# Optimization experiments

Measured on AMD Instinct MI355X. Metric: run time of the kernel, lower is better.

Reference implementation:

```python
import jax, jax.numpy as jnp
import numpy as np

N = 50000   # nodes
E = 400000  # edges
IN = 64     # input feature dim
H = 4       # heads (layers 1-2)
C = 128     # hidden channels per head
NEG_SLOPE = 0.2


def gat_conv(x, W, a_src, a_dst, b, src, dst, num_nodes):
    """PyG-style GATConv (add_self_loops=False, dropout inactive / eval mode).
    x: [N, F_in]; W: [F_in, H*C]; a_src/a_dst: [H, C]; b: [H*C].
    Returns concat-over-heads output [N, H*C]."""
    h = (x @ W).reshape(num_nodes, a_src.shape[0], a_src.shape[1])  # [N,H,C]
    alpha_s = jnp.einsum('nhc,hc->nh', h, a_src)  # [N,H]
    alpha_d = jnp.einsum('nhc,hc->nh', h, a_dst)  # [N,H]
    e = jax.nn.leaky_relu(alpha_s[src] + alpha_d[dst], NEG_SLOPE)  # [E,H]
    # numerically-stable segment softmax over incoming edges of each dst node
    m = jax.ops.segment_max(e, dst, num_segments=num_nodes)       # [N,H]
    m = jnp.where(jnp.isfinite(m), m, 0.0)                        # empty segments
    p = jnp.exp(e - m[dst])                                       # [E,H]
    denom = jax.ops.segment_sum(p, dst, num_segments=num_nodes)   # [N,H]
    alpha = p / (denom[dst] + 1e-16)                              # [E,H]
    # message = alpha * h[src], scatter-add into dst
    out = jax.ops.segment_sum(alpha[:, :, None] * h[src], dst,
                              num_segments=num_nodes)             # [N,H,C]
    return out.reshape(num_nodes, -1) + b


def setup_inputs() -> dict:
    key = jax.random.key(0)
    ks = jax.random.split(key, 16)
    s = 0.1  # weight scale for stability
    inp = {
        'x': jax.random.normal(ks[0], (N, IN), dtype=jnp.float32),
        'edge_index': jax.random.randint(ks[1], (2, E), 0, N, dtype=jnp.int64),
        # layer 1: 64 -> H*C
        'W1': s * jax.random.normal(ks[2], (IN, H * C), dtype=jnp.float32),
        'a_src1': s * jax.random.normal(ks[3], (H, C), dtype=jnp.float32),
        'a_dst1': s * jax.random.normal(ks[4], (H, C), dtype=jnp.float32),
        'b1': jnp.zeros((H * C,), dtype=jnp.float32),
        # layer 2: H*C -> H*C
        'W2': s * jax.random.normal(ks[5], (H * C, H * C), dtype=jnp.float32),
        'a_src2': s * jax.random.normal(ks[6], (H, C), dtype=jnp.float32),
        'a_dst2': s * jax.random.normal(ks[7], (H, C), dtype=jnp.float32),
        'b2': jnp.zeros((H * C,), dtype=jnp.float32),
        # layer 3: H*C -> C (heads=1)
        'W3': s * jax.random.normal(ks[8], (H * C, C), dtype=jnp.float32),
        'a_src3': s * jax.random.normal(ks[9], (1, C), dtype=jnp.float32),
        'a_dst3': s * jax.random.normal(ks[10], (1, C), dtype=jnp.float32),
        'b3': jnp.zeros((C,), dtype=jnp.float32),
    }
    return inp


def reference(x, edge_index, W1, a_src1, a_dst1, b1, W2, a_src2, a_dst2, b2,
              W3, a_src3, a_dst3, b3):
    src, dst = edge_index[0], edge_index[1]
    h = jax.nn.elu(gat_conv(x, W1, a_src1, a_dst1, b1, src, dst, N))
    h = jax.nn.elu(gat_conv(h, W2, a_src2, a_dst2, b2, src, dst, N))
    h = jax.nn.elu(gat_conv(h, W3, a_src3, a_dst3, b3, src, dst, N))
    return h  # [N, C]
```

## Files before the change

### kernel.cpp

```cpp
#include <hip/hip_runtime.h>
#include <math.h>


#define LRELU_SLOPE 0.2f
#define MPAD 50048

typedef __attribute__((ext_vector_type(8))) short short8;
typedef __attribute__((ext_vector_type(4))) float f32x4;

__device__ __forceinline__ float bf2f(unsigned short u) {
    return __uint_as_float(((unsigned int)u) << 16);
}
__device__ __forceinline__ unsigned short f2bf(float f) {
    unsigned int u = __float_as_uint(f);
    unsigned int r = u + 0x7FFFu + ((u >> 16) & 1u);
    return (unsigned short)(r >> 16);
}
__device__ __forceinline__ void load16_to_lds(const void* g, void* l) {
    __builtin_amdgcn_global_load_lds(
        (const __attribute__((address_space(1))) void*)g,
        (__attribute__((address_space(3))) void*)l, 16, 0, 0);
}
__device__ __forceinline__ float lrelu(float e) {
    return e > 0.f ? e : LRELU_SLOPE * e;
}


__global__ __launch_bounds__(256) void prep_kernel(
    const float* __restrict__ x, const float* __restrict__ W1,
    const float* __restrict__ W2, const float* __restrict__ W3,
    unsigned short* __restrict__ x_bf, unsigned short* __restrict__ W1t,
    unsigned short* __restrict__ W2t, unsigned short* __restrict__ W3t,
    int* __restrict__ counts, int N)
{
    int i = blockIdx.x * 256 + threadIdx.x;
    const int nx = N * 64;
    if (i < nx) { x_bf[i] = f2bf(x[i]); return; }
    i -= nx;
    if (i < 64 * 512) {
        int k = i / 512, nn = i % 512;
        W1t[nn * 64 + k] = f2bf(W1[i]);
        return;
    }
    i -= 64 * 512;
    if (i < 512 * 512) {
        int k = i / 512, nn = i % 512;
        W2t[nn * 512 + k] = f2bf(W2[i]);
        return;
    }
    i -= 512 * 512;
    if (i < 512 * 128) {
        int k = i / 128, nn = i % 128;
        W3t[(size_t)nn * 512 + k] = f2bf(W3[i]);
        return;
    }
    i -= 512 * 128;
    if (i < N) counts[i] = 0;
}


__global__ void count_deg_kernel(const int* __restrict__ dst, int* __restrict__ counts, int E) {
    int e = blockIdx.x * blockDim.x + threadIdx.x;
    if (e < E) atomicAdd(&counts[dst[e]], 1);
}

__global__ __launch_bounds__(1024) void scan1_kernel(const int* __restrict__ counts,
                                                     int* __restrict__ row_ptr,
                                                     int* __restrict__ partial, int n) {
    __shared__ int wsum[16];
    const int t = threadIdx.x;
    const int lane = t & 63, w = t >> 6;
    const int i = blockIdx.x * 1024 + t;
    int v = (i < n) ? counts[i] : 0;
    int s = v;
    #pragma unroll
    for (int off = 1; off < 64; off <<= 1) {
        int u = __shfl_up(s, off);
        if (lane >= off) s += u;
    }
    if (lane == 63) wsum[w] = s;
    __syncthreads();
    if (w == 0 && lane < 16) {
        int tv = wsum[lane];
        #pragma unroll
        for (int off = 1; off < 16; off <<= 1) {
            int u = __shfl_up(tv, off);
            if (lane >= off) tv += u;
        }
        wsum[lane] = tv;
    }
    __syncthreads();
    int incl = s + (w > 0 ? wsum[w - 1] : 0);
    if (i < n) row_ptr[i + 1] = incl;
    if (t == 0) partial[blockIdx.x] = wsum[15];
}

__global__ void scan2_kernel(int* __restrict__ partial, int nb) {
    int lane = threadIdx.x;
    int v = (lane < nb) ? partial[lane] : 0;
    int s = v;
    #pragma unroll
    for (int off = 1; off < 64; off <<= 1) {
        int u = __shfl_up(s, off);
        if (lane >= off) s += u;
    }
    if (lane < nb) partial[lane] = s - v;
}

__global__ __launch_bounds__(1024) void scan3c_kernel(int* __restrict__ row_ptr,
                                                      const int* __restrict__ partial,
                                                      const int* __restrict__ counts,
                                                      int* __restrict__ cursor, int n) {
    const int i = blockIdx.x * 1024 + threadIdx.x;
    if (i < n) {
        int rp1 = row_ptr[i + 1] + partial[blockIdx.x];
        row_ptr[i + 1] = rp1;
        cursor[i] = rp1 - counts[i];
    }
    if (i == 0) row_ptr[0] = 0;
}

__global__ void fill_csr_kernel(const int* __restrict__ src, const int* __restrict__ dst,
                                int* __restrict__ cursor, int* __restrict__ csr_src, int E) {
    int e = blockIdx.x * blockDim.x + threadIdx.x;
    if (e < E) {
        int d = dst[e];
        int pos = atomicAdd(&cursor[d], 1);
        csr_src[pos] = src[e];
    }
}


__global__ __launch_bounds__(256) void gemm_mfma_kernel(
    const unsigned short* __restrict__ A,
    const unsigned short* __restrict__ Bt,
    unsigned short* __restrict__ C,
    const float* __restrict__ a_src,
    const float* __restrict__ a_dst,
    float* __restrict__ als,
    float* __restrict__ ald,
    int M, int N, int K, int H)
{
    __shared__ short As[2 * 128 * 32];
    __shared__ short Bs[2 * 128 * 32];
    const int t = threadIdx.x;
    const int w = t >> 6, lane = t & 63;
    const int wr = w >> 1, wc = w & 1;

    const int nwg = gridDim.x * gridDim.y;
    const int wg  = blockIdx.x + gridDim.x * blockIdx.y;
    const int qch = nwg >> 3, rch = nwg & 7;
    const int xcd = wg & 7, pos = wg >> 3;
    const int lg  = (xcd < rch ? xcd * (qch + 1) : rch * (qch + 1) + (xcd - rch) * qch) + pos;
    const int bx  = lg % gridDim.x;
    const int by  = lg / gridDim.x;

    const int rowBase = by * 128;
    const int colBase = bx * 128;
    const int q = lane >> 4;
    const int r16 = lane & 15;
    const int qs = (q ^ ((r16 >> 1) & 3)) * 8;

    f32x4 acc[4][4] = {};

    const int sRow = t >> 2;
    const int sOff = ((t & 3) ^ ((sRow >> 1) & 3)) * 8;

    const int NT = K >> 5;
    auto stage = [&](int kt, int b) {
        const int koff = kt * 32 + sOff;
        #pragma unroll
        for (int rr = 0; rr < 2; ++rr) {
            const unsigned short* gA = A + (size_t)(rowBase + rr * 64 + sRow) * K + koff;
            load16_to_lds(gA, (char*)As + b * 8192 + rr * 4096 + w * 1024);
            const unsigned short* gB = Bt + (size_t)(colBase + rr * 64 + sRow) * K + koff;
            load16_to_lds(gB, (char*)Bs + b * 8192 + rr * 4096 + w * 1024);
        }
    };

    stage(0, 0);
    __syncthreads();

    for (int kt = 0; kt < NT; ++kt) {
        const int cur = kt & 1;
        if (kt + 1 < NT) stage(kt + 1, cur ^ 1);

        const short* Ab = As + cur * 4096;
        const short* Bb = Bs + cur * 4096;
        short8 af[4], bfr[4];
        #pragma unroll
        for (int m = 0; m < 4; ++m)
            af[m] = *(const short8*)&Ab[(wr * 64 + m * 16 + r16) * 32 + qs];
        #pragma unroll
        for (int n = 0; n < 4; ++n)
            bfr[n] = *(const short8*)&Bb[(wc * 64 + n * 16 + r16) * 32 + qs];
        #pragma unroll
        for (int m = 0; m < 4; ++m)
            #pragma unroll
            for (int n = 0; n < 4; ++n)
                acc[m][n] = __builtin_amdgcn_mfma_f32_16x16x32_bf16(af[m], bfr[n], acc[m][n], 0, 0, 0);

        __syncthreads();
    }

    float asv[4], adv[4];
    #pragma unroll
    for (int n = 0; n < 4; ++n) {
        int col = colBase + wc * 64 + n * 16 + r16;
        asv[n] = a_src[col];
        adv[n] = a_dst[col];
    }
    const int head = bx;

    float* red = (float*)As;

    #pragma unroll
    for (int m = 0; m < 4; ++m) {
        #pragma unroll
        for (int r = 0; r < 4; ++r) {
            const int rowl = wr * 64 + m * 16 + q * 4 + r;
            const int gr = rowBase + rowl;
            float ps = 0.f, pd = 0.f;
            #pragma unroll
            for (int n = 0; n < 4; ++n) {
                ps += acc[m][n][r] * asv[n];
                pd += acc[m][n][r] * adv[n];
            }
            #pragma unroll
            for (int off = 8; off >= 1; off >>= 1) {
                ps += __shfl_xor(ps, off);
                pd += __shfl_xor(pd, off);
            }
            if (r16 == 0) {
                red[wc * 128 + rowl] = ps;
                red[256 + wc * 128 + rowl] = pd;
            }
            if (gr < M) {
                #pragma unroll
                for (int n = 0; n < 4; ++n)
                    C[(size_t)gr * N + colBase + wc * 64 + n * 16 + r16] = f2bf(acc[m][n][r]);
            }
        }
    }
    __syncthreads();
    if (t < 128) {
        const int gr = rowBase + t;
        if (gr < M) {
            als[(size_t)gr * H + head] = red[t] + red[128 + t];
            ald[(size_t)gr * H + head] = red[256 + t] + red[384 + t];
        }
    }
}


__global__ __launch_bounds__(256) void gather4f_kernel(
    const unsigned short* __restrict__ hfeat,
    const float* __restrict__ als, const float* __restrict__ ald,
    const int* __restrict__ row_ptr, const int* __restrict__ csr_src,
    const float* __restrict__ bias, unsigned short* __restrict__ out,
    int n_nodes)
{
    const int lane = threadIdx.x & 63;
    const int wv = threadIdx.x >> 6;
    const int n = blockIdx.x * 4 + wv;
    if (n >= n_nodes) return;
    const int head = lane >> 4;
    const int li = lane & 15;
    const int grpBase = lane & ~15;

    const int start = row_ptr[n];
    const int deg = row_ptr[n + 1] - start;
    const float aldv = ald[(size_t)n * 4 + head];

    float acc[8] = {};
    float wsum = 0.f;
    for (int base = 0; base < deg; base += 16) {
        const int cnt = min(16, deg - base);
        int s_l = 0; float w_l = 0.f;
        if (li < cnt) {
            s_l = csr_src[start + base + li];
            float e = als[(size_t)s_l * 4 + head] + aldv;
            w_l = __expf(lrelu(e));
            wsum += w_l;
        }
        for (int e = 0; e < cnt; ++e) {
            const int s = __shfl(s_l, grpBase + e);
            const float a = __shfl(w_l, grpBase + e);
            short8 v = *(const short8*)(hfeat + (size_t)s * 512 + lane * 8);
            #pragma unroll
            for (int j = 0; j < 8; ++j) acc[j] += a * bf2f((unsigned short)v[j]);
        }
    }

    #pragma unroll
    for (int off = 8; off >= 1; off >>= 1) wsum += __shfl_xor(wsum, off);
    const float sc = (deg > 0) ? 1.f / wsum : 0.f;

    float ov[8];
    #pragma unroll
    for (int j = 0; j < 8; ++j) {
        float o = acc[j] * sc + bias[lane * 8 + j];
        ov[j] = o > 0.f ? o : expm1f(o);
    }
    short8 v;
    #pragma unroll
    for (int j = 0; j < 8; ++j) v[j] = (short)f2bf(ov[j]);
    *(short8*)&out[(size_t)n * 512 + lane * 8] = v;
}


__global__ __launch_bounds__(256) void gather1f_kernel(
    const unsigned short* __restrict__ hfeat,
    const float* __restrict__ als, const float* __restrict__ ald,
    const int* __restrict__ row_ptr, const int* __restrict__ csr_src,
    const float* __restrict__ bias, float* __restrict__ out, int n_nodes)
{
    const int lane = threadIdx.x & 63;
    const int wv = threadIdx.x >> 6;
    const int n = blockIdx.x * 4 + wv;
    if (n >= n_nodes) return;
    const int qid = lane >> 4;
    const int ql = lane & 15;

    const int start = row_ptr[n];
    const int deg = row_ptr[n + 1] - start;
    const float aldv = ald[n];

    float acc[8] = {};
    float wsum = 0.f;
    for (int base = 0; base < deg; base += 64) {
        const int cnt = min(64, deg - base);
        int s_l = 0; float w_l = 0.f;
        if (lane < cnt) {
            s_l = csr_src[start + base + lane];
            float e = als[s_l] + aldv;
            w_l = __expf(lrelu(e));
            wsum += w_l;
        }
        for (int e = 0; e < cnt; e += 4) {
            const int idx = e + qid;
            const int idxc = idx < cnt ? idx : 0;
            const int s = __shfl(s_l, idxc);
            const float aw = __shfl(w_l, idxc);
            const float a = idx < cnt ? aw : 0.f;
            short8 v = *(const short8*)(hfeat + (size_t)s * 128 + ql * 8);
            #pragma unroll
            for (int j = 0; j < 8; ++j) acc[j] += a * bf2f((unsigned short)v[j]);
        }
    }

    #pragma unroll
    for (int off = 32; off >= 1; off >>= 1) wsum += __shfl_xor(wsum, off);
    const float sc = (deg > 0) ? 1.f / wsum : 0.f;

    #pragma unroll
    for (int j = 0; j < 8; ++j) {
        acc[j] += __shfl_xor(acc[j], 16);
        acc[j] += __shfl_xor(acc[j], 32);
    }

    if (qid == 0) {
        float tmp[8];
        #pragma unroll
        for (int j = 0; j < 8; ++j) {
            float o = acc[j] * sc + bias[ql * 8 + j];
            tmp[j] = o > 0.f ? o : expm1f(o);
        }
        float4 o0 = {tmp[0], tmp[1], tmp[2], tmp[3]};
        float4 o1 = {tmp[4], tmp[5], tmp[6], tmp[7]};
        float* op = out + (size_t)n * 128 + ql * 8;
        *(float4*)op = o0;
        *(float4*)(op + 4) = o1;
    }
}


extern "C" void kernel_launch(void* const* d_in, const int* in_sizes, int n_in,
                              void* d_out, int out_size, void* d_ws, size_t ws_size,
                              hipStream_t stream) {
    const float* x   = (const float*)d_in[0];
    const int*   ei  = (const int*)d_in[1];
    const float* W1  = (const float*)d_in[2];
    const float* as1 = (const float*)d_in[3];
    const float* ad1 = (const float*)d_in[4];
    const float* b1  = (const float*)d_in[5];
    const float* W2  = (const float*)d_in[6];
    const float* as2 = (const float*)d_in[7];
    const float* ad2 = (const float*)d_in[8];
    const float* b2  = (const float*)d_in[9];
    const float* W3  = (const float*)d_in[10];
    const float* as3 = (const float*)d_in[11];
    const float* ad3 = (const float*)d_in[12];
    const float* b3  = (const float*)d_in[13];

    const int N = in_sizes[0] / 64;
    const int E = in_sizes[1] / 2;
    const int HC = 512;

    const int* src = ei;
    const int* dst = ei + E;

    size_t off = 0;
    auto carve = [&](size_t bytes) -> void* {
        void* p = (char*)d_ws + off;
        off += (bytes + 255) & ~(size_t)255;
        return p;
    };
    unsigned short* x_bf    = (unsigned short*)carve((size_t)MPAD * 64 * 2);
    unsigned short* feat_bf = (unsigned short*)carve((size_t)MPAD * HC * 2);
    unsigned short* h_bf    = (unsigned short*)carve((size_t)N * HC * 2);
    unsigned short* W1t     = (unsigned short*)carve((size_t)512 * 64 * 2);
    unsigned short* W2t     = (unsigned short*)carve((size_t)512 * 512 * 2);
    unsigned short* W3t     = (unsigned short*)carve((size_t)128 * 512 * 2);
    float* stats  = (float*)carve((size_t)N * 8 * sizeof(float));
    float* als    = stats;
    float* ald    = stats + (size_t)N * 4;
    int*   counts = (int*)carve((size_t)N * sizeof(int));
    int*   row_ptr= (int*)carve((size_t)(N + 1) * sizeof(int));
    int*   cursor = (int*)carve((size_t)N * sizeof(int));
    int*   csr_src= (int*)carve((size_t)E * sizeof(int));
    int*   partial= (int*)carve(64 * sizeof(int));
    (void)ws_size;

    const int nb = (N + 1023) / 1024;
    const int prepTotal = N * 64 + 64 * 512 + 512 * 512 + 512 * 128 + N;

    prep_kernel<<<(prepTotal + 255) / 256, 256, 0, stream>>>(
        x, W1, W2, W3, x_bf, W1t, W2t, W3t, counts, N);

    count_deg_kernel<<<(E + 255) / 256, 256, 0, stream>>>(dst, counts, E);
    scan1_kernel<<<nb, 1024, 0, stream>>>(counts, row_ptr, partial, N);
    scan2_kernel<<<1, 64, 0, stream>>>(partial, nb);
    scan3c_kernel<<<nb, 1024, 0, stream>>>(row_ptr, partial, counts, cursor, N);
    fill_csr_kernel<<<(E + 255) / 256, 256, 0, stream>>>(src, dst, cursor, csr_src, E);

    const int rowTiles = (N + 127) / 128;
    const int aggBlocks = (N + 3) / 4;

    gemm_mfma_kernel<<<dim3(4, rowTiles), 256, 0, stream>>>(x_bf, W1t, h_bf, as1, ad1,
                                                            als, ald, N, 512, 64, 4);
    gather4f_kernel<<<aggBlocks, 256, 0, stream>>>(h_bf, als, ald, row_ptr, csr_src,
                                                   b1, feat_bf, N);

    gemm_mfma_kernel<<<dim3(4, rowTiles), 256, 0, stream>>>(feat_bf, W2t, h_bf, as2, ad2,
                                                            als, ald, N, 512, 512, 4);
    gather4f_kernel<<<aggBlocks, 256, 0, stream>>>(h_bf, als, ald, row_ptr, csr_src,
                                                   b2, feat_bf, N);

    gemm_mfma_kernel<<<dim3(1, rowTiles), 256, 0, stream>>>(feat_bf, W3t, h_bf, as3, ad3,
                                                            als, ald, N, 128, 512, 1);
    gather1f_kernel<<<aggBlocks, 256, 0, stream>>>(h_bf, als, ald, row_ptr, csr_src,
                                                   b3, (float*)d_out, N);
}
```

Measured before the change: 359.4 us.

## Reorder layer-1 GAT to aggregate 64-dim inputs before projecting through W1

```diff
diff --git a/kernel.cpp b/kernel.cpp
--- a/kernel.cpp
+++ b/kernel.cpp
@@ -8,8 +8,8 @@
 typedef __attribute__((ext_vector_type(8))) short short8;
 typedef __attribute__((ext_vector_type(4))) float f32x4;
 
-__device__ __forceinline__ float bf2f(unsigned short u) {
-    return __uint_as_float(((unsigned int)u) << 16);
+__device__ __forceinline__ float bf2f(unsigned int u) {
+    return __uint_as_float(u << 16);
 }
 __device__ __forceinline__ unsigned short f2bf(float f) {
     unsigned int u = __float_as_uint(f);
@@ -29,9 +29,10 @@
 __global__ __launch_bounds__(256) void prep_kernel(
     const float* __restrict__ x, const float* __restrict__ W1,
     const float* __restrict__ W2, const float* __restrict__ W3,
+    const float* __restrict__ as1, const float* __restrict__ ad1,
     unsigned short* __restrict__ x_bf, unsigned short* __restrict__ W1t,
     unsigned short* __restrict__ W2t, unsigned short* __restrict__ W3t,
-    int* __restrict__ counts, int N)
+    int* __restrict__ counts, float* __restrict__ ws, int N)
 {
     int i = blockIdx.x * 256 + threadIdx.x;
     const int nx = N * 64;
@@ -55,7 +56,19 @@
         return;
     }
     i -= 512 * 128;
-    if (i < N) counts[i] = 0;
+    if (i < N) { counts[i] = 0; return; }
+    i -= N;
+    if (i < 256) {
+        int h = i >> 6, k = i & 63;
+        float ss = 0.f, sd = 0.f;
+        for (int c = 0; c < 128; ++c) {
+            float wv = W1[k * 512 + h * 128 + c];
+            ss += wv * as1[h * 128 + c];
+            sd += wv * ad1[h * 128 + c];
+        }
+        ws[i] = ss;
+        ws[256 + i] = sd;
+    }
 }
 
 
@@ -127,6 +140,178 @@
         int d = dst[e];
         int pos = atomicAdd(&cursor[d], 1);
         csr_src[pos] = src[e];
+    }
+}
+
+
+__global__ __launch_bounds__(256) void als1_kernel(const float* __restrict__ x,
+                                                   const float* __restrict__ ws,
+                                                   float* __restrict__ als,
+                                                   float* __restrict__ ald, int n_nodes) {
+    const int lane = threadIdx.x & 63;
+    const int wv = threadIdx.x >> 6;
+    const int n = blockIdx.x * 4 + wv;
+    if (n >= n_nodes) return;
+    const float xv = x[(size_t)n * 64 + lane];
+    float d0 = xv * ws[lane],        d1 = xv * ws[64 + lane];
+    float d2 = xv * ws[128 + lane],  d3 = xv * ws[192 + lane];
+    float e0 = xv * ws[256 + lane],  e1 = xv * ws[320 + lane];
+    float e2 = xv * ws[384 + lane],  e3 = xv * ws[448 + lane];
+    #pragma unroll
+    for (int off = 32; off >= 1; off >>= 1) {
+        d0 += __shfl_xor(d0, off); d1 += __shfl_xor(d1, off);
+        d2 += __shfl_xor(d2, off); d3 += __shfl_xor(d3, off);
+        e0 += __shfl_xor(e0, off); e1 += __shfl_xor(e1, off);
+        e2 += __shfl_xor(e2, off); e3 += __shfl_xor(e3, off);
+    }
+    if (lane == 0) {
+        float4 a = {d0, d1, d2, d3};
+        float4 b = {e0, e1, e2, e3};
+        *(float4*)&als[(size_t)n * 4] = a;
+        *(float4*)&ald[(size_t)n * 4] = b;
+    }
+}
+
+
+__global__ __launch_bounds__(256) void gatherx_kernel(
+    const unsigned short* __restrict__ x_bf,
+    const float* __restrict__ als, const float* __restrict__ ald,
+    const int* __restrict__ row_ptr, const int* __restrict__ csr_src,
+    unsigned short* __restrict__ xagg,
+    int n_nodes)
+{
+    const int lane = threadIdx.x & 63;
+    const int wv = threadIdx.x >> 6;
+    const int n = blockIdx.x * 4 + wv;
+    if (n >= n_nodes) return;
+    const int head = lane >> 4;
+    const int li = lane & 15;
+    const int grpBase = lane & ~15;
+
+    const int start = row_ptr[n];
+    const int deg = row_ptr[n + 1] - start;
+    const float aldv = ald[(size_t)n * 4 + head];
+
+    float acc[4] = {};
+    float wsum = 0.f;
+    for (int base = 0; base < deg; base += 16) {
+        const int cnt = min(16, deg - base);
+        int s_l = 0; float w_l = 0.f;
+        if (li < cnt) {
+            s_l = csr_src[start + base + li];
+            w_l = __expf(lrelu(als[(size_t)s_l * 4 + head] + aldv));
+            wsum += w_l;
+        }
+        for (int e = 0; e < cnt; ++e) {
+            const int s = __shfl(s_l, grpBase + e);
+            const float a = __shfl(w_l, grpBase + e);
+            uint2 v = *(const uint2*)(x_bf + (size_t)s * 64 + li * 4);
+            acc[0] += a * bf2f(v.x & 0xFFFFu);
+            acc[1] += a * bf2f(v.x >> 16);
+            acc[2] += a * bf2f(v.y & 0xFFFFu);
+            acc[3] += a * bf2f(v.y >> 16);
+        }
+    }
+
+    #pragma unroll
+    for (int off = 8; off >= 1; off >>= 1) wsum += __shfl_xor(wsum, off);
+    const float sc = (deg > 0) ? 1.f / wsum : 0.f;
+
+    uint2 o;
+    o.x = (unsigned int)f2bf(acc[0] * sc) | ((unsigned int)f2bf(acc[1] * sc) << 16);
+    o.y = (unsigned int)f2bf(acc[2] * sc) | ((unsigned int)f2bf(acc[3] * sc) << 16);
+    *(uint2*)&xagg[(size_t)n * 256 + head * 64 + li * 4] = o;
+}
+
+
+__global__ __launch_bounds__(256) void gemm_out_kernel(
+    const unsigned short* __restrict__ A,
+    const unsigned short* __restrict__ Bt,
+    const float* __restrict__ bias,
+    unsigned short* __restrict__ Cout,
+    int M)
+{
+    __shared__ short As[2 * 128 * 32];
+    __shared__ short Bs[2 * 128 * 32];
+    const int t = threadIdx.x;
+    const int w = t >> 6, lane = t & 63;
+    const int wr = w >> 1, wc = w & 1;
+
+    const int nwg = gridDim.x * gridDim.y;
+    const int wg  = blockIdx.x + gridDim.x * blockIdx.y;
+    const int qch = nwg >> 3, rch = nwg & 7;
+    const int xcd = wg & 7, pos = wg >> 3;
+    const int lg  = (xcd < rch ? xcd * (qch + 1) : rch * (qch + 1) + (xcd - rch) * qch) + pos;
+    const int bx  = lg % gridDim.x;
+    const int by  = lg / gridDim.x;
+
+    const int rowBase = by * 128;
+    const int head = bx;
+    const int colBase = bx * 128;
+    const int q = lane >> 4;
+    const int r16 = lane & 15;
+    const int qs = (q ^ ((r16 >> 1) & 3)) * 8;
+
+    f32x4 acc[4][4] = {};
+
+    const int sRow = t >> 2;
+    const int sOff = ((t & 3) ^ ((sRow >> 1) & 3)) * 8;
+
+    auto stage = [&](int kt, int b) {
+        const int koff = kt * 32 + sOff;
+        #pragma unroll
+        for (int rr = 0; rr < 2; ++rr) {
+            const unsigned short* gA = A + (size_t)(rowBase + rr * 64 + sRow) * 256 + head * 64 + koff;
+            load16_to_lds(gA, (char*)As + b * 8192 + rr * 4096 + w * 1024);
+            const unsigned short* gB = Bt + (size_t)(colBase + rr * 64 + sRow) * 64 + koff;
+            load16_to_lds(gB, (char*)Bs + b * 8192 + rr * 4096 + w * 1024);
+        }
+    };
+
+    stage(0, 0);
+    __syncthreads();
+
+    #pragma unroll
+    for (int kt = 0; kt < 2; ++kt) {
+        const int cur = kt & 1;
+        if (kt + 1 < 2) stage(kt + 1, cur ^ 1);
+
+        const short* Ab = As + cur * 4096;
+        const short* Bb = Bs + cur * 4096;
+        short8 af[4], bfr[4];
+        #pragma unroll
+        for (int m = 0; m < 4; ++m)
+            af[m] = *(const short8*)&Ab[(wr * 64 + m * 16 + r16) * 32 + qs];
+        #pragma unroll
+        for (int n = 0; n < 4; ++n)
+            bfr[n] = *(const short8*)&Bb[(wc * 64 + n * 16 + r16) * 32 + qs];
+        #pragma unroll
+        for (int m = 0; m < 4; ++m)
+            #pragma unroll
+            for (int n = 0; n < 4; ++n)
+                acc[m][n] = __builtin_amdgcn_mfma_f32_16x16x32_bf16(af[m], bfr[n], acc[m][n], 0, 0, 0);
+
+        __syncthreads();
+    }
+
+    float bv[4];
+    #pragma unroll
+    for (int n = 0; n < 4; ++n) bv[n] = bias[colBase + wc * 64 + n * 16 + r16];
+
+    #pragma unroll
+    for (int m = 0; m < 4; ++m) {
+        #pragma unroll
+        for (int r = 0; r < 4; ++r) {
+            const int gr = rowBase + wr * 64 + m * 16 + q * 4 + r;
+            if (gr < M) {
+                #pragma unroll
+                for (int n = 0; n < 4; ++n) {
+                    float o = acc[m][n][r] + bv[n];
+                    o = o > 0.f ? o : expm1f(o);
+                    Cout[(size_t)gr * 512 + colBase + wc * 64 + n * 16 + r16] = f2bf(o);
+                }
+            }
+        }
     }
 }
 
@@ -288,7 +473,7 @@
             const float a = __shfl(w_l, grpBase + e);
             short8 v = *(const short8*)(hfeat + (size_t)s * 512 + lane * 8);
             #pragma unroll
-            for (int j = 0; j < 8; ++j) acc[j] += a * bf2f((unsigned short)v[j]);
+            for (int j = 0; j < 8; ++j) acc[j] += a * bf2f((unsigned int)(unsigned short)v[j]);
         }
     }
 
@@ -345,7 +530,7 @@
             const float a = idx < cnt ? aw : 0.f;
             short8 v = *(const short8*)(hfeat + (size_t)s * 128 + ql * 8);
             #pragma unroll
-            for (int j = 0; j < 8; ++j) acc[j] += a * bf2f((unsigned short)v[j]);
+            for (int j = 0; j < 8; ++j) acc[j] += a * bf2f((unsigned int)(unsigned short)v[j]);
         }
     }
 
@@ -409,12 +594,14 @@
     unsigned short* x_bf    = (unsigned short*)carve((size_t)MPAD * 64 * 2);
     unsigned short* feat_bf = (unsigned short*)carve((size_t)MPAD * HC * 2);
     unsigned short* h_bf    = (unsigned short*)carve((size_t)N * HC * 2);
+    unsigned short* xagg    = (unsigned short*)carve((size_t)MPAD * 256 * 2);
     unsigned short* W1t     = (unsigned short*)carve((size_t)512 * 64 * 2);
     unsigned short* W2t     = (unsigned short*)carve((size_t)512 * 512 * 2);
     unsigned short* W3t     = (unsigned short*)carve((size_t)128 * 512 * 2);
     float* stats  = (float*)carve((size_t)N * 8 * sizeof(float));
     float* als    = stats;
     float* ald    = stats + (size_t)N * 4;
+    float* ws     = (float*)carve(512 * sizeof(float) * 2);
     int*   counts = (int*)carve((size_t)N * sizeof(int));
     int*   row_ptr= (int*)carve((size_t)(N + 1) * sizeof(int));
     int*   cursor = (int*)carve((size_t)N * sizeof(int));
@@ -423,10 +610,10 @@
     (void)ws_size;
 
     const int nb = (N + 1023) / 1024;
-    const int prepTotal = N * 64 + 64 * 512 + 512 * 512 + 512 * 128 + N;
+    const int prepTotal = N * 64 + 64 * 512 + 512 * 512 + 512 * 128 + N + 256;
 
     prep_kernel<<<(prepTotal + 255) / 256, 256, 0, stream>>>(
-        x, W1, W2, W3, x_bf, W1t, W2t, W3t, counts, N);
+        x, W1, W2, W3, as1, ad1, x_bf, W1t, W2t, W3t, counts, ws, N);
 
     count_deg_kernel<<<(E + 255) / 256, 256, 0, stream>>>(dst, counts, E);
     scan1_kernel<<<nb, 1024, 0, stream>>>(counts, row_ptr, partial, N);
@@ -437,10 +624,9 @@
     const int rowTiles = (N + 127) / 128;
     const int aggBlocks = (N + 3) / 4;
 
-    gemm_mfma_kernel<<<dim3(4, rowTiles), 256, 0, stream>>>(x_bf, W1t, h_bf, as1, ad1,
-                                                            als, ald, N, 512, 64, 4);
-    gather4f_kernel<<<aggBlocks, 256, 0, stream>>>(h_bf, als, ald, row_ptr, csr_src,
-                                                   b1, feat_bf, N);
+    als1_kernel<<<aggBlocks, 256, 0, stream>>>(x, ws, als, ald, N);
+    gatherx_kernel<<<aggBlocks, 256, 0, stream>>>(x_bf, als, ald, row_ptr, csr_src, xagg, N);
+    gemm_out_kernel<<<dim3(4, rowTiles), 256, 0, stream>>>(xagg, W1t, b1, feat_bf, N);
 
     gemm_mfma_kernel<<<dim3(4, rowTiles), 256, 0, stream>>>(feat_bf, W2t, h_bf, as2, ad2,
                                                             als, ald, N, 512, 512, 4);
```

New measurement: 350.6 us. -2.4%, faster.
